# Performance work log

Hardware: AMD Instinct MI355X
Metric: run time of the kernel (lower is better)

## Reference

```python
import jax, jax.numpy as jnp
import numpy as np

K = 3
STRIDE = 1
PAD = 1
CHUNK = 8  # matches torch chunking over output channels; keeps diff tensor small


def _ringify(x):
    # map angles to (-pi, pi]
    return (x + np.pi) % (2.0 * np.pi) - np.pi


def _unfold(x, k, stride, pad):
    """torch F.unfold equivalent. x:(B,C,H,W) -> (B, C*k*k, L), plus (Ho, Wo)."""
    B, C, H, W = x.shape
    xp = jnp.pad(x, ((0, 0), (0, 0), (pad, pad), (pad, pad)))
    Hp, Wp = H + 2 * pad, W + 2 * pad
    Ho = (Hp - k) // stride + 1
    Wo = (Wp - k) // stride + 1
    cols = []
    for i in range(k):
        for j in range(k):
            cols.append(xp[:, :, i:i + stride * Ho:stride, j:j + stride * Wo:stride])
    p = jnp.stack(cols, axis=2)  # (B, C, k*k, Ho, Wo) -> matches unfold's (C, kh, kw) order
    return p.reshape(B, C * k * k, Ho * Wo), Ho, Wo


def setup_inputs() -> dict:
    key = jax.random.key(0)
    k1, k2 = jax.random.split(key)
    x = jax.random.normal(k1, (4, 32, 64, 64), dtype=jnp.float32)
    weight = jax.random.normal(k2, (64, 32, K, K), dtype=jnp.float32)
    return {"x": x, "weight": weight}


def reference(x, weight):
    B, C, H, W = x.shape
    O = weight.shape[0]
    patches, Ho, Wo = _unfold(x, K, STRIDE, PAD)  # (B, P, L)
    P = C * K * K
    w_chunks = weight.reshape(O, P).reshape(O // CHUNK, CHUNK, P)

    def body(carry, wf):  # wf: (CHUNK, P)
        diff = _ringify(patches[:, None, :, :] - wf[None, :, :, None])  # (B, CHUNK, P, L)
        dir_x = jnp.cos(diff).sum(axis=2)
        dir_y = jnp.sin(diff).sum(axis=2)
        return carry, jnp.arctan2(dir_y, dir_x)  # (B, CHUNK, L)

    _, outs = jax.lax.scan(body, None, w_chunks)  # (O//CHUNK, B, CHUNK, L)
    out = jnp.moveaxis(outs, 0, 1).reshape(B, O, Ho, Wo)
    return out
```

## Files before the change

kernel.cpp:

```cpp
#include <hip/hip_runtime.h>
#include <math.h>


typedef float f32x4 __attribute__((ext_vector_type(4)));
typedef _Float16 f16;
typedef f16 f16x2 __attribute__((ext_vector_type(2)));
typedef f16 f16x8 __attribute__((ext_vector_type(8)));
typedef unsigned int u32;
typedef u32 u32x4 __attribute__((ext_vector_type(4)));

#define B_   4
#define C_   32
#define H_   64
#define W_   64
#define O_   64
#define HW   (H_ * W_)
#define NPIX (B_ * C_ * HW)
#define KP   24
#define PLANES_BYTES (NPIX * 4)
#define BSW_ELEMS (8 * KP * 64 * 8)
#define BSW_BYTES (BSW_ELEMS * 2)
#define NEED_WS ((size_t)PLANES_BYTES + (size_t)BSW_BYTES)

__global__ __launch_bounds__(256) void ring_prep(const float* __restrict__ x,
                                                 const float* __restrict__ w,
                                                 u32* __restrict__ planes,
                                                 f16* __restrict__ bsw) {
    const int bid = blockIdx.x, tid = threadIdx.x;
    if (bid < 512) {
        int i = bid * 256 + tid;
        f32x4 xv = ((const f32x4*)x)[i];
        u32x4 pk;
#pragma unroll
        for (int j = 0; j < 4; ++j) {
            float s, cc;
            __sincosf(xv[j], &s, &cc);
            f16x2 h = {(f16)cc, (f16)s};
            pk[j] = __builtin_bit_cast(u32, h);
        }
        ((u32x4*)planes)[i] = pk;
    } else {
        int idx = (bid - 512) * 256 + tid;
        int nf   = idx / 12288;
        int rem  = idx % 12288;
        int ks   = rem >> 9;
        int rem2 = rem & 511;
        int lane = rem2 >> 3;
        int e    = rem2 & 7;
        int k = ks * 32 + (lane >> 4) * 8 + e;
        int n = nf * 16 + (lane & 15);
        int q = k >> 1, t = k & 1;
        int j  = q & 3;
        int ri = q >> 2;
        int c  = ri / 3, i3 = ri - 3 * (ri / 3);
        f16 val = (f16)0.f;
        if (j < 3) {
            int o = n & 63;
            float s, cc;
            __sincosf(w[(o * C_ + c) * 9 + i3 * 3 + j], &s, &cc);
            float v = (n < 64) ? (t ? s : cc) : (t ? cc : -s);
            val = (f16)v;
        }
        bsw[idx] = val;
    }
}

__global__ __launch_bounds__(256, 2) void ring_mfma(const u32* __restrict__ planes,
                                                    const f16* __restrict__ bsw,
                                                    float* __restrict__ out) {
    __shared__ u32 sm[C_ * 10 * 12];

    const int tid = threadIdx.x;
    const int tile = blockIdx.x;
    const int TY = (tile >> 3) * 8;
    const int TX = (tile & 7) * 8;
    const int half = blockIdx.y;
    const int b = blockIdx.z;

    const u32* pb = planes + (size_t)b * C_ * HW;
#pragma unroll 1
    for (int i = tid; i < C_ * 120; i += 256) {
        int c  = i / 120;
        int rm = i % 120;
        int rr = rm / 12;
        int cc = rm % 12;
        int gh = TY + rr - 1;
        int gw = TX + cc - 1;
        u32 v = 0x00003C00u;
        if ((unsigned)gh < (unsigned)H_ && (unsigned)gw < (unsigned)W_)
            v = pb[c * HW + gh * W_ + gw];
        sm[i] = v;
    }
    __syncthreads();

    const int wv = tid >> 6;
    const int l  = tid & 63;
    const int g  = l >> 4;
    const int lr = l & 15;
    const int p  = wv * 16 + lr;
    const int py = p >> 3, px = p & 7;

    const u32x4* bv = (const u32x4*)bsw;
    int ofs0 = (2 * half + 0) * KP * 64 + l;
    int ofs1 = (2 * half + 1) * KP * 64 + l;
    int ofs2 = (4 + 2 * half) * KP * 64 + l;
    int ofs3 = (5 + 2 * half) * KP * 64 + l;

    f32x4 acc0 = {0.f, 0.f, 0.f, 0.f}, acc1 = acc0, acc2 = acc0, acc3 = acc0;

#pragma unroll 2
    for (int ks = 0; ks < KP; ++ks) {
        int ri = ks * 4 + g;
        int c  = ri / 3;
        int i3 = ri - 3 * c;
        int base = c * 120 + (py + i3) * 12 + px;
        u32x4 au = {sm[base], sm[base + 1], sm[base + 2], sm[base + 3]};
        f16x8 af = __builtin_bit_cast(f16x8, au);
        f16x8 b0 = __builtin_bit_cast(f16x8, bv[ofs0 + ks * 64]);
        f16x8 b1 = __builtin_bit_cast(f16x8, bv[ofs1 + ks * 64]);
        f16x8 b2 = __builtin_bit_cast(f16x8, bv[ofs2 + ks * 64]);
        f16x8 b3 = __builtin_bit_cast(f16x8, bv[ofs3 + ks * 64]);
        acc0 = __builtin_amdgcn_mfma_f32_16x16x32_f16(af, b0, acc0, 0, 0, 0);
        acc1 = __builtin_amdgcn_mfma_f32_16x16x32_f16(af, b1, acc1, 0, 0, 0);
        acc2 = __builtin_amdgcn_mfma_f32_16x16x32_f16(af, b2, acc2, 0, 0, 0);
        acc3 = __builtin_amdgcn_mfma_f32_16x16x32_f16(af, b3, acc3, 0, 0, 0);
    }

#pragma unroll
    for (int r = 0; r < 4; ++r) {
        int p2 = wv * 16 + g * 4 + r;
        int h  = TY + (p2 >> 3);
        int wc = TX + (p2 & 7);
        int o0 = half * 32 + lr;
        out[((size_t)(b * O_ + o0) * HW) + h * W_ + wc] = atan2f(acc2[r], acc0[r]);
        out[((size_t)(b * O_ + o0 + 16) * HW) + h * W_ + wc] = atan2f(acc3[r], acc1[r]);
    }
}

typedef float f32x2 __attribute__((ext_vector_type(2)));
#define FOC 4
#define FCG 8
__global__ __launch_bounds__(256, 4) void ring_fb(const float* __restrict__ x,
                                                  const float* __restrict__ w,
                                                  float* __restrict__ out) {
    __shared__ f32x2 sm2[FCG][18][18];
    __shared__ f32x4 wsm[C_][9][FOC / 2];
    const int tid = threadIdx.x;
    const int tile = blockIdx.x;
    const int tile_y = (tile >> 2) * 16, tile_x = (tile & 3) * 16;
    const int ob = blockIdx.y * FOC;
    const int b = blockIdx.z;
#pragma unroll 1
    for (int i = tid; i < C_ * 9 * FOC; i += 256) {
        int c = i / (9 * FOC), rest = i % (9 * FOC);
        int ij = rest >> 2, oo = rest & 3;
        float s, cc;
        __sincosf(w[(ob + oo) * (C_ * 9) + c * 9 + ij], &s, &cc);
        float* dst = (float*)&wsm[c][ij][oo >> 1];
        dst[(oo & 1) * 2 + 0] = cc;
        dst[(oo & 1) * 2 + 1] = s;
    }
    const int ty = tid >> 4, tx = tid & 15;
    float ax[FOC], ay[FOC];
#pragma unroll
    for (int o = 0; o < FOC; ++o) { ax[o] = 0.f; ay[o] = 0.f; }
    const float* xb = x + (size_t)b * C_ * HW;
    for (int cg = 0; cg < C_; cg += FCG) {
        __syncthreads();
#pragma unroll 1
        for (int i = tid; i < FCG * 324; i += 256) {
            int c = i / 324, rr = i % 324, r = rr / 18, cl = rr % 18;
            int hh = tile_y + r - 1, ww = tile_x + cl - 1;
            f32x2 v = (f32x2){1.f, 0.f};
            if ((unsigned)hh < (unsigned)H_ && (unsigned)ww < (unsigned)W_) {
                float s, cc;
                __sincosf(xb[(cg + c) * HW + hh * W_ + ww], &s, &cc);
                v = (f32x2){cc, s};
            }
            sm2[c][r][cl] = v;
        }
        __syncthreads();
#pragma unroll 2
        for (int c = 0; c < FCG; ++c) {
            f32x2 P[9];
#pragma unroll
            for (int i = 0; i < 3; ++i)
#pragma unroll
                for (int j = 0; j < 3; ++j) P[i * 3 + j] = sm2[c][ty + i][tx + j];
            const f32x4* wp = &wsm[cg + c][0][0];
#pragma unroll
            for (int ij = 0; ij < 9; ++ij) {
                f32x4 w0 = wp[ij * 2 + 0], w1 = wp[ij * 2 + 1];
                float cx = P[ij].x, sx = P[ij].y;
                ax[0] = fmaf(cx, w0.x, fmaf(sx, w0.y, ax[0]));
                ay[0] = fmaf(sx, w0.x, fmaf(-cx, w0.y, ay[0]));
                ax[1] = fmaf(cx, w0.z, fmaf(sx, w0.w, ax[1]));
                ay[1] = fmaf(sx, w0.z, fmaf(-cx, w0.w, ay[1]));
                ax[2] = fmaf(cx, w1.x, fmaf(sx, w1.y, ax[2]));
                ay[2] = fmaf(sx, w1.x, fmaf(-cx, w1.y, ay[2]));
                ax[3] = fmaf(cx, w1.z, fmaf(sx, w1.w, ax[3]));
                ay[3] = fmaf(sx, w1.z, fmaf(-cx, w1.w, ay[3]));
            }
        }
    }
    const int h = tile_y + ty, wc = tile_x + tx;
    float* op = out + (size_t)(b * O_ + ob) * HW + h * W_ + wc;
#pragma unroll
    for (int o = 0; o < FOC; ++o) op[(size_t)o * HW] = atan2f(ay[o], ax[o]);
}

extern "C" void kernel_launch(void* const* d_in, const int* in_sizes, int n_in,
                              void* d_out, int out_size, void* d_ws, size_t ws_size,
                              hipStream_t stream) {
    const float* x = (const float*)d_in[0];
    const float* w = (const float*)d_in[1];
    float* out = (float*)d_out;

    if (ws_size >= NEED_WS) {
        u32* planes = (u32*)d_ws;
        f16* bsw = (f16*)((char*)d_ws + PLANES_BYTES);
        ring_prep<<<dim3(512 + 384), dim3(256), 0, stream>>>(x, w, planes, bsw);
        dim3 grid(64, 2, B_);
        ring_mfma<<<grid, dim3(256), 0, stream>>>(planes, bsw, out);
    } else {
        dim3 grid(16, O_ / FOC, B_);
        ring_fb<<<grid, dim3(256), 0, stream>>>(x, w, out);
    }
}
```

Measured before the change: 75.81 us.

## Split MFMA kernel across four output-channel quarters with software-prefetched operands

The grid now splits output channels into four 16-channel quarters instead of two halves, so each block runs two MFMA accumulators rather than four and twice as many blocks launch. The shared-memory tile is padded to 128 entries per channel so the fill loop uses shifts and a fixed trip count. The K loop double-buffers the LDS A-fragment and global B-fragment loads one step ahead, and the launch bound is raised to allow four blocks per CU. The extra blocks mean the halo tile is loaded from global memory twice as often and the per-block shared fill is repeated.

```diff
diff --git a/kernel.cpp b/kernel.cpp
--- a/kernel.cpp
+++ b/kernel.cpp
@@ -65,30 +65,33 @@
     }
 }
 
-__global__ __launch_bounds__(256, 2) void ring_mfma(const u32* __restrict__ planes,
+__global__ __launch_bounds__(256, 4) void ring_mfma(const u32* __restrict__ planes,
                                                     const f16* __restrict__ bsw,
                                                     float* __restrict__ out) {
-    __shared__ u32 sm[C_ * 10 * 12];
+    __shared__ u32 sm[C_ * 128];
 
     const int tid = threadIdx.x;
     const int tile = blockIdx.x;
     const int TY = (tile >> 3) * 8;
     const int TX = (tile & 7) * 8;
-    const int half = blockIdx.y;
+    const int q4 = blockIdx.y;
     const int b = blockIdx.z;
 
     const u32* pb = planes + (size_t)b * C_ * HW;
 #pragma unroll 1
-    for (int i = tid; i < C_ * 120; i += 256) {
-        int c  = i / 120;
-        int rm = i % 120;
-        int rr = rm / 12;
-        int cc = rm % 12;
-        int gh = TY + rr - 1;
-        int gw = TX + cc - 1;
+    for (int it = 0; it < 16; ++it) {
+        int i  = it * 256 + tid;
+        int rm = i & 127;
         u32 v = 0x00003C00u;
-        if ((unsigned)gh < (unsigned)H_ && (unsigned)gw < (unsigned)W_)
-            v = pb[c * HW + gh * W_ + gw];
+        if (rm < 120) {
+            int c  = i >> 7;
+            int rr = rm / 12;
+            int cl = rm - rr * 12;
+            int gh = TY + rr - 1;
+            int gw = TX + cl - 1;
+            if ((unsigned)gh < (unsigned)H_ && (unsigned)gw < (unsigned)W_)
+                v = pb[c * HW + gh * W_ + gw];
+        }
         sm[i] = v;
     }
     __syncthreads();
@@ -98,42 +101,47 @@
     const int g  = l >> 4;
     const int lr = l & 15;
     const int p  = wv * 16 + lr;
-    const int py = p >> 3, px = p & 7;
+    const int py12 = (p >> 3) * 12;
+    const int px = p & 7;
 
     const u32x4* bv = (const u32x4*)bsw;
-    int ofs0 = (2 * half + 0) * KP * 64 + l;
-    int ofs1 = (2 * half + 1) * KP * 64 + l;
-    int ofs2 = (4 + 2 * half) * KP * 64 + l;
-    int ofs3 = (5 + 2 * half) * KP * 64 + l;
-
-    f32x4 acc0 = {0.f, 0.f, 0.f, 0.f}, acc1 = acc0, acc2 = acc0, acc3 = acc0;
-
-#pragma unroll 2
-    for (int ks = 0; ks < KP; ++ks) {
+    const int ofs0 = q4 * (KP * 64) + l;
+    const int ofs1 = (4 + q4) * (KP * 64) + l;
+
+    f32x4 acc0 = {0.f, 0.f, 0.f, 0.f}, acc1 = acc0;
+
+    auto ldA = [&](int ks) -> u32x4 {
         int ri = ks * 4 + g;
         int c  = ri / 3;
         int i3 = ri - 3 * c;
-        int base = c * 120 + (py + i3) * 12 + px;
-        u32x4 au = {sm[base], sm[base + 1], sm[base + 2], sm[base + 3]};
-        f16x8 af = __builtin_bit_cast(f16x8, au);
-        f16x8 b0 = __builtin_bit_cast(f16x8, bv[ofs0 + ks * 64]);
-        f16x8 b1 = __builtin_bit_cast(f16x8, bv[ofs1 + ks * 64]);
-        f16x8 b2 = __builtin_bit_cast(f16x8, bv[ofs2 + ks * 64]);
-        f16x8 b3 = __builtin_bit_cast(f16x8, bv[ofs3 + ks * 64]);
-        acc0 = __builtin_amdgcn_mfma_f32_16x16x32_f16(af, b0, acc0, 0, 0, 0);
-        acc1 = __builtin_amdgcn_mfma_f32_16x16x32_f16(af, b1, acc1, 0, 0, 0);
-        acc2 = __builtin_amdgcn_mfma_f32_16x16x32_f16(af, b2, acc2, 0, 0, 0);
-        acc3 = __builtin_amdgcn_mfma_f32_16x16x32_f16(af, b3, acc3, 0, 0, 0);
-    }
-
+        int base = (c << 7) + py12 + i3 * 12 + px;
+        return (u32x4){sm[base], sm[base + 1], sm[base + 2], sm[base + 3]};
+    };
+
+    u32x4 a_c = ldA(0);
+    u32x4 b0_c = bv[ofs0];
+    u32x4 b1_c = bv[ofs1];
+
+#pragma unroll 4
+    for (int ks = 0; ks < KP; ++ks) {
+        int ksn = (ks + 1 < KP) ? ks + 1 : ks;
+        u32x4 a_n  = ldA(ksn);
+        u32x4 b0_n = bv[ofs0 + ksn * 64];
+        u32x4 b1_n = bv[ofs1 + ksn * 64];
+        f16x8 af = __builtin_bit_cast(f16x8, a_c);
+        acc0 = __builtin_amdgcn_mfma_f32_16x16x32_f16(af, __builtin_bit_cast(f16x8, b0_c), acc0, 0, 0, 0);
+        acc1 = __builtin_amdgcn_mfma_f32_16x16x32_f16(af, __builtin_bit_cast(f16x8, b1_c), acc1, 0, 0, 0);
+        a_c = a_n; b0_c = b0_n; b1_c = b1_n;
+    }
+
+    const int o = q4 * 16 + lr;
+    float* ob = out + (size_t)(b * O_ + o) * HW;
 #pragma unroll
     for (int r = 0; r < 4; ++r) {
         int p2 = wv * 16 + g * 4 + r;
         int h  = TY + (p2 >> 3);
         int wc = TX + (p2 & 7);
-        int o0 = half * 32 + lr;
-        out[((size_t)(b * O_ + o0) * HW) + h * W_ + wc] = atan2f(acc2[r], acc0[r]);
-        out[((size_t)(b * O_ + o0 + 16) * HW) + h * W_ + wc] = atan2f(acc3[r], acc1[r]);
+        ob[h * W_ + wc] = atan2f(acc1[r], acc0[r]);
     }
 }
 
@@ -220,7 +228,7 @@
         u32* planes = (u32*)d_ws;
         f16* bsw = (f16*)((char*)d_ws + PLANES_BYTES);
         ring_prep<<<dim3(512 + 384), dim3(256), 0, stream>>>(x, w, planes, bsw);
-        dim3 grid(64, 2, B_);
+        dim3 grid(64, 4, B_);
         ring_mfma<<<grid, dim3(256), 0, stream>>>(planes, bsw, out);
     } else {
         dim3 grid(16, O_ / FOC, B_);
```

Result: faster. 72.11 us (-4.9%).
